# Kernel tuning notes

Hardware: AMD Instinct MI355X
Metric: run time of the kernel (lower is better)

## Reference

```python
import jax, jax.numpy as jnp
import numpy as np

B, N, D, D_OUT = 8, 2048, 256, 256
LN_EPS = 1e-5
LRELU_SLOPE = 0.01


def setup_inputs() -> dict:
    key = jax.random.key(0)
    ks = jax.random.split(key, 11)
    s_in = 1.0 / np.sqrt(D)
    s_out = 1.0 / np.sqrt(D)
    return {
        "x_local": jax.random.normal(ks[0], (B, N, D), dtype=jnp.float32),
        "Wq": jax.random.uniform(ks[1], (D, D), jnp.float32, -s_in, s_in),
        "bq": jax.random.uniform(ks[2], (D,), jnp.float32, -s_in, s_in),
        "Wk": jax.random.uniform(ks[3], (D, D), jnp.float32, -s_in, s_in),
        "bk": jax.random.uniform(ks[4], (D,), jnp.float32, -s_in, s_in),
        "Wv": jax.random.uniform(ks[5], (D, D), jnp.float32, -s_in, s_in),
        "bv": jax.random.uniform(ks[6], (D,), jnp.float32, -s_in, s_in),
        "Wo": jax.random.uniform(ks[7], (D_OUT, D), jnp.float32, -s_out, s_out),
        "bo": jax.random.uniform(ks[8], (D_OUT,), jnp.float32, -s_out, s_out),
        "ln_gamma": jnp.ones((D_OUT,), jnp.float32),
        "ln_beta": jnp.zeros((D_OUT,), jnp.float32),
    }


def reference(x_local, Wq, bq, Wk, bk, Wv, bv, Wo, bo, ln_gamma, ln_beta):
    # Linear layers (torch convention: y = x @ W.T + b)
    Q = jnp.einsum("bnd,ed->bne", x_local, Wq) + bq
    K = jnp.einsum("bnd,ed->bne", x_local, Wk) + bk
    V = jnp.einsum("bnd,ed->bne", x_local, Wv) + bv
    # Unscaled attention (source applies no 1/sqrt(d))
    scores = jnp.einsum("bnd,bmd->bnm", Q, K)          # [B, N, N]
    attn = jax.nn.softmax(scores, axis=-1)
    loc = jnp.einsum("bnm,bmd->bnd", attn, V)           # [B, N, D]
    # fc_out: Linear -> LayerNorm -> LeakyReLU
    h = jnp.einsum("bnd,ed->bne", loc, Wo) + bo          # [B, N, D_OUT]
    mu = jnp.mean(h, axis=-1, keepdims=True)
    var = jnp.mean(jnp.square(h - mu), axis=-1, keepdims=True)
    hn = (h - mu) / jnp.sqrt(var + LN_EPS) * ln_gamma + ln_beta
    return jnp.where(hn >= 0, hn, LRELU_SLOPE * hn)
```

## Files before the change

kernel.cpp:

```cpp
#include <hip/hip_runtime.h>

typedef unsigned short u16;
typedef __attribute__((ext_vector_type(8))) _Float16 f16x8;
typedef __attribute__((ext_vector_type(4))) float f32x4;

#define MFMA_F16 __builtin_amdgcn_mfma_f32_16x16x32_f16

static __device__ __forceinline__ u16 f2h(float f) {
    return __builtin_bit_cast(u16, (_Float16)f);
}
static __device__ __forceinline__ ushort4 f4_to_h4(const float4 v) {
    ushort4 r;
    r.x = f2h(v.x); r.y = f2h(v.y); r.z = f2h(v.z); r.w = f2h(v.w);
    return r;
}
static __device__ __forceinline__ void gl16(const u16* g, u16* l) {
    __builtin_amdgcn_global_load_lds(
        (__attribute__((address_space(1))) void*)(g),
        (__attribute__((address_space(3))) void*)(l),
        16, 0, 0);
}

__global__ __launch_bounds__(256) void prep_w(
    const float* __restrict__ wq, const float* __restrict__ wk,
    const float* __restrict__ wv, const float* __restrict__ wo,
    u16* __restrict__ w4)
{
    const int tid = blockIdx.x * 256 + threadIdx.x;
    for (int i = tid; i < 65536; i += 16384) {
        const float* src = (i < 16384) ? wq : (i < 32768) ? wk
                         : (i < 49152) ? wv : wo;
        ((ushort4*)w4)[i] = f4_to_h4(((const float4*)src)[i & 16383]);
    }
}

__global__ __launch_bounds__(256, 3) void proj_qkv(
    const float* __restrict__ X, const u16* __restrict__ w4,
    const float* __restrict__ bq, const float* __restrict__ bk,
    const float* __restrict__ bv,
    u16* __restrict__ Qh, u16* __restrict__ Kh, u16* __restrict__ Vt)
{
    const int z = blockIdx.y;
    const u16* __restrict__ W     = w4 + z * 65536;
    const float* __restrict__ bias = (z == 0) ? bq : (z == 1) ? bk : bv;

    const int m0   = blockIdx.x * 64;
    const int t    = threadIdx.x;
    const int w    = t >> 6;
    const int lane = t & 63;
    const int quad = lane >> 4;
    const int l16  = lane & 15;

    __shared__ __align__(16) u16 smem[18432];
    u16* Xs = smem;
    u16* Ws = smem + 2560;

    f32x4 acc[16];
#pragma unroll
    for (int i = 0; i < 16; ++i) acc[i] = f32x4{0.f, 0.f, 0.f, 0.f};

    for (int kc = 0; kc < 8; ++kc) {
#pragma unroll
        for (int i = 0; i < 2; ++i) {
            const int ch = i * 256 + t;
            const int row = ch >> 3, cg = ch & 7;
            const float4 v = *(const float4*)&X[(size_t)(m0 + row) * 256 + kc * 32 + cg * 4];
            *(ushort4*)&Xs[row * 40 + cg * 4] = f4_to_h4(v);
        }
#pragma unroll
        for (int i = 0; i < 4; ++i) {
            const int ch = i * 256 + t;
            const int row = ch >> 2, cg = ch & 3;
            *(int4*)&Ws[row * 40 + cg * 8] =
                *(const int4*)&W[(size_t)row * 256 + kc * 32 + cg * 8];
        }
        __syncthreads();

        const f16x8 af = *(const f16x8*)&Xs[(w * 16 + l16) * 40 + quad * 8];
#pragma unroll
        for (int nt = 0; nt < 16; ++nt) {
            const f16x8 bf = *(const f16x8*)&Ws[(nt * 16 + l16) * 40 + quad * 8];
            acc[nt] = MFMA_F16(af, bf, acc[nt], 0, 0, 0);
        }
        __syncthreads();
    }

    if (z < 2) {
        u16* __restrict__ Y = (z == 0) ? Qh : Kh;
#pragma unroll
        for (int nt = 0; nt < 16; ++nt) {
            const int col = nt * 16 + l16;
            const float bb = bias[col];
#pragma unroll
            for (int r = 0; r < 4; ++r)
                smem[(w * 16 + quad * 4 + r) * 264 + col] = f2h(acc[nt][r] + bb);
        }
        __syncthreads();
#pragma unroll
        for (int i = 0; i < 8; ++i) {
            const int ch = i * 256 + t;
            const int row = ch >> 5, cg = ch & 31;
            *(int4*)&Y[(size_t)(m0 + row) * 256 + cg * 8] =
                *(const int4*)&smem[row * 264 + cg * 8];
        }
    } else {
        const int b  = m0 >> 11;
        const int n0 = m0 & 2047;
#pragma unroll
        for (int nt = 0; nt < 16; ++nt) {
            const int col = nt * 16 + l16;
            const float bb = bias[col];
            ushort4 h4;
            h4.x = f2h(acc[nt][0] + bb);
            h4.y = f2h(acc[nt][1] + bb);
            h4.z = f2h(acc[nt][2] + bb);
            h4.w = f2h(acc[nt][3] + bb);
            *(ushort4*)&smem[col * 72 + w * 16 + quad * 4] = h4;
        }
        __syncthreads();
#pragma unroll
        for (int i = 0; i < 8; ++i) {
            const int ch = i * 256 + t;
            const int row = ch >> 3, cg = ch & 7;
            *(int4*)&Vt[(size_t)b * 524288 + (size_t)row * 2048 + n0 + cg * 8] =
                *(const int4*)&smem[row * 72 + cg * 8];
        }
    }
}

__global__ __launch_bounds__(256, 2) void attn(
    const u16* __restrict__ Qh, const u16* __restrict__ Kg,
    const u16* __restrict__ Vt, u16* __restrict__ Op, float* __restrict__ lmp)
{
    const int nz = gridDim.z;
    const int z  = blockIdx.z;
    const int ntiles = 32;
    const int tile0  = ntiles * z;

    const int b  = blockIdx.y;
    const int q0 = blockIdx.x * 64;
    const int t    = threadIdx.x;
    const int w    = t >> 6;
    const int lane = t & 63;
    const int quad = lane >> 4;
    const int l16  = lane & 15;

    __shared__ __align__(16) u16 smem[32768];
    u16* Os = smem;

    f16x8 qf[8];
    {
        const size_t qrow = (size_t)(b * 2048 + q0 + w * 16 + l16) * 256;
#pragma unroll
        for (int kc = 0; kc < 8; ++kc)
            qf[kc] = *(const f16x8*)&Qh[qrow + kc * 32 + quad * 8];
    }

    unsigned kgb[4], vgb[4];
#pragma unroll
    for (int i = 0; i < 4; ++i) {
        const int j  = w * 4 + i;
        const int r  = 2 * j + (lane >> 5);
        const int pr = ((r >> 2) & 3) * 8 + (r >> 4) * 4 + (r & 3);
        const int c  = lane & 31;
        kgb[i] = (unsigned)((b * 2048 + pr) * 256 + ((c ^ (r & 7)) * 8));
        const int rp = 8 * j + (lane >> 3);
        const int c8 = lane & 7;
        const int d  = 2 * rp + (c8 >> 2);
        const int a  = (c8 & 3) ^ (rp & 3);
        vgb[i] = (unsigned)(b * 524288 + d * 2048 + a * 8);
    }

#define STAGE(bufsel, kt_) do {                                              \
        u16* Kb_ = smem + (bufsel) * 16384;                                  \
        u16* Vb_ = Kb_ + 8192;                                               \
        _Pragma("unroll")                                                    \
        for (int i_ = 0; i_ < 4; ++i_) {                                     \
            gl16(Kg + kgb[i_] + (unsigned)(kt_) * 256,                       \
                 Kb_ + (w * 4 + i_) * 512);                                  \
            gl16(Vt + vgb[i_] + (unsigned)(kt_),                             \
                 Vb_ + (w * 4 + i_) * 512);                                  \
        }                                                                    \
    } while (0)

    f32x4 O[16];
#pragma unroll
    for (int i = 0; i < 16; ++i) O[i] = f32x4{0.f, 0.f, 0.f, 0.f};
    float mrow = -1e30f, lrow = 0.f;

    const int vbase = (l16 >> 1) * 64 + (l16 & 1) * 32
                    + ((quad ^ ((l16 >> 1) & 3)) * 8);

    STAGE(0, tile0 * 32);

    for (int it = 0; it < ntiles; ++it) {
        asm volatile("s_waitcnt vmcnt(0)" ::: "memory");
        __builtin_amdgcn_s_barrier();
        __builtin_amdgcn_sched_barrier(0);
        if (it + 1 < ntiles) STAGE((it + 1) & 1, (tile0 + it + 1) * 32);
        __builtin_amdgcn_sched_barrier(0);

        const u16* Kc = smem + (it & 1) * 16384;
        const u16* Vc = Kc + 8192;

        f32x4 S[2];
        S[0] = f32x4{0.f, 0.f, 0.f, 0.f};
        S[1] = f32x4{0.f, 0.f, 0.f, 0.f};
        __builtin_amdgcn_s_setprio(1);
#pragma unroll
        for (int kc = 0; kc < 8; ++kc) {
#pragma unroll
            for (int kn = 0; kn < 2; ++kn) {
                const int r2 = kn * 16 + l16;
                const f16x8 kf = *(const f16x8*)
                    &Kc[r2 * 256 + (((kc * 4 + quad) ^ (l16 & 7)) * 8)];
                S[kn] = MFMA_F16(kf, qf[kc], S[kn], 0, 0, 0);
            }
        }
        __builtin_amdgcn_s_setprio(0);

        float mt = fmaxf(fmaxf(fmaxf(S[0][0], S[0][1]), fmaxf(S[0][2], S[0][3])),
                         fmaxf(fmaxf(S[1][0], S[1][1]), fmaxf(S[1][2], S[1][3])));
        mt = fmaxf(mt, __shfl_xor(mt, 16));
        mt = fmaxf(mt, __shfl_xor(mt, 32));
        if (__any(mt - mrow > 8.f)) {
            const float mnew = fmaxf(mrow, mt);
            const float a = __expf(mrow - mnew);
            lrow *= a;
#pragma unroll
            for (int dv = 0; dv < 16; ++dv)
#pragma unroll
                for (int r = 0; r < 4; ++r) O[dv][r] *= a;
            mrow = mnew;
        }
        f16x8 pfv;
        float s = 0.f;
#pragma unroll
        for (int kn = 0; kn < 2; ++kn)
#pragma unroll
            for (int r = 0; r < 4; ++r) {
                const float e = __expf(S[kn][r] - mrow);
                s += e;
                pfv[kn * 4 + r] = (_Float16)e;
            }
        s += __shfl_xor(s, 16);
        s += __shfl_xor(s, 32);
        lrow += s;

        __builtin_amdgcn_s_setprio(1);
#pragma unroll
        for (int dvt = 0; dvt < 16; ++dvt) {
            const f16x8 vf = *(const f16x8*)&Vc[dvt * 512 + vbase];
            O[dvt] = MFMA_F16(vf, pfv, O[dvt], 0, 0, 0);
        }
        __builtin_amdgcn_s_setprio(0);
    }
#undef STAGE

    __syncthreads();
    {
        const float rl = 1.0f / lrow;
#pragma unroll
        for (int dvt = 0; dvt < 16; ++dvt) {
            ushort4 h4;
            h4.x = f2h(O[dvt][0] * rl);
            h4.y = f2h(O[dvt][1] * rl);
            h4.z = f2h(O[dvt][2] * rl);
            h4.w = f2h(O[dvt][3] * rl);
            *(ushort4*)&Os[(w * 16 + l16) * 264 + dvt * 16 + quad * 4] = h4;
        }
        if (quad == 0) {
            const int grow = b * 2048 + q0 + w * 16 + l16;
            lmp[z * 16384 + grow]        = lrow;
            lmp[(nz + z) * 16384 + grow] = mrow;
        }
    }
    __syncthreads();

    u16* __restrict__ Oz = Op + (size_t)z * 4194304;
    {
        const int row = t >> 2;
#pragma unroll
        for (int i = 0; i < 8; ++i) {
            const int chunk = (t & 3) * 8 + i;
            *(int4*)&Oz[(size_t)(b * 2048 + q0 + row) * 256 + chunk * 8] =
                *(const int4*)&Os[row * 264 + chunk * 8];
        }
    }
}

__global__ __launch_bounds__(256, 2) void outproj_ln(
    const u16* __restrict__ Op, const float* __restrict__ lmp,
    const u16* __restrict__ Woh, const float* __restrict__ bo,
    const float* __restrict__ gamma, const float* __restrict__ beta,
    float* __restrict__ out)
{
    const int m0   = blockIdx.x * 32;
    const int t    = threadIdx.x;
    const int w    = t >> 6;
    const int rw   = w & 1;
    const int cw   = w >> 1;
    const int lane = t & 63;
    const int quad = lane >> 4;
    const int l16  = lane & 15;

    __shared__ __align__(16) u16 Ls[32 * 40];
    __shared__ __align__(16) u16 Ws[256 * 40];
    __shared__ _Float16 wls[2][32];
    __shared__ float part[2][16][2][2];

    if (t < 32) {
        const float l0 = lmp[m0 + t],          l1 = lmp[16384 + m0 + t];
        const float mm0 = lmp[32768 + m0 + t], mm1 = lmp[49152 + m0 + t];
        const float mm = fmaxf(mm0, mm1);
        const float u0 = l0 * __expf(mm0 - mm);
        const float u1 = l1 * __expf(mm1 - mm);
        const float inv = 1.0f / (u0 + u1);
        wls[0][t] = (_Float16)(u0 * inv);
        wls[1][t] = (_Float16)(u1 * inv);
    }
    __syncthreads();

    f32x4 acc[8];
#pragma unroll
    for (int i = 0; i < 8; ++i) acc[i] = f32x4{0.f, 0.f, 0.f, 0.f};

    for (int kc = 0; kc < 8; ++kc) {
        if (t < 128) {
            const int row = t >> 2, cg = t & 3;
            const size_t off = (size_t)(m0 + row) * 256 + kc * 32 + cg * 8;
            const f16x8 o0 = __builtin_bit_cast(f16x8, *(const int4*)&Op[off]);
            const f16x8 o1 = __builtin_bit_cast(f16x8, *(const int4*)&Op[4194304 + off]);
            const _Float16 w0 = wls[0][row], w1 = wls[1][row];
            f16x8 lw;
#pragma unroll
            for (int j = 0; j < 8; ++j) lw[j] = o0[j] * w0 + o1[j] * w1;
            *(int4*)&Ls[row * 40 + cg * 8] = __builtin_bit_cast(int4, lw);
        }
#pragma unroll
        for (int i = 0; i < 4; ++i) {
            const int ch = i * 256 + t;
            const int row = ch >> 2, cg = ch & 3;
            *(int4*)&Ws[row * 40 + cg * 8] =
                *(const int4*)&Woh[(size_t)row * 256 + kc * 32 + cg * 8];
        }
        __syncthreads();

        const f16x8 af = *(const f16x8*)&Ls[(rw * 16 + l16) * 40 + quad * 8];
#pragma unroll
        for (int nt = 0; nt < 8; ++nt) {
            const f16x8 bf = *(const f16x8*)&Ws[((cw * 8 + nt) * 16 + l16) * 40 + quad * 8];
            acc[nt] = MFMA_F16(af, bf, acc[nt], 0, 0, 0);
        }
        __syncthreads();
    }

    float g[8], bt[8], bb[8];
#pragma unroll
    for (int nt = 0; nt < 8; ++nt) {
        const int col = cw * 128 + nt * 16 + l16;
        bb[nt] = bo[col]; g[nt] = gamma[col]; bt[nt] = beta[col];
    }

    float shv[4], sh2v[4];
#pragma unroll
    for (int r = 0; r < 4; ++r) {
        float sh = 0.f, sh2 = 0.f;
#pragma unroll
        for (int nt = 0; nt < 8; ++nt) {
            const float h = acc[nt][r] + bb[nt];
            sh  += h;
            sh2 += h * h;
        }
        sh  += __shfl_xor(sh, 1);  sh  += __shfl_xor(sh, 2);
        sh  += __shfl_xor(sh, 4);  sh  += __shfl_xor(sh, 8);
        sh2 += __shfl_xor(sh2, 1); sh2 += __shfl_xor(sh2, 2);
        sh2 += __shfl_xor(sh2, 4); sh2 += __shfl_xor(sh2, 8);
        shv[r] = sh; sh2v[r] = sh2;
    }
    if (l16 == 0) {
#pragma unroll
        for (int r = 0; r < 4; ++r) {
            part[rw][quad * 4 + r][cw][0] = shv[r];
            part[rw][quad * 4 + r][cw][1] = sh2v[r];
        }
    }
    __syncthreads();

#pragma unroll
    for (int r = 0; r < 4; ++r) {
        const float sh  = shv[r]  + part[rw][quad * 4 + r][cw ^ 1][0];
        const float sh2 = sh2v[r] + part[rw][quad * 4 + r][cw ^ 1][1];
        const float mu  = sh * (1.f / 256.f);
        const float var = fmaxf(sh2 * (1.f / 256.f) - mu * mu, 0.f);
        const float rs  = rsqrtf(var + 1e-5f);
        const size_t row = (size_t)(m0 + rw * 16 + quad * 4 + r) * 256;
#pragma unroll
        for (int nt = 0; nt < 8; ++nt) {
            const float hn = (acc[nt][r] + bb[nt] - mu) * rs * g[nt] + bt[nt];
            out[row + cw * 128 + nt * 16 + l16] = (hn >= 0.f) ? hn : 0.01f * hn;
        }
    }
}

extern "C" void kernel_launch(void* const* d_in, const int* in_sizes, int n_in,
                              void* d_out, int out_size, void* d_ws, size_t ws_size,
                              hipStream_t stream)
{
    const float* x  = (const float*)d_in[0];
    const float* Wq = (const float*)d_in[1];
    const float* bq = (const float*)d_in[2];
    const float* Wk = (const float*)d_in[3];
    const float* bk = (const float*)d_in[4];
    const float* Wv = (const float*)d_in[5];
    const float* bv = (const float*)d_in[6];
    const float* Wo = (const float*)d_in[7];
    const float* bo = (const float*)d_in[8];
    const float* gm = (const float*)d_in[9];
    const float* bt = (const float*)d_in[10];
    float* out = (float*)d_out;

    u16* W4 = (u16*)d_ws;
    u16* Qh = W4 + 262144;
    u16* Kh = Qh + 4194304;
    u16* Vt = Kh + 4194304;
    u16* Op = Vt + 4194304;
    float* lmp = (float*)(Op + 2 * 4194304);
    u16* Woh = W4 + 196608;

    prep_w     <<<64,             256, 0, stream>>>(Wq, Wk, Wv, Wo, W4);
    proj_qkv   <<<dim3(256, 3),   256, 0, stream>>>(x, W4, bq, bk, bv, Qh, Kh, Vt);
    attn       <<<dim3(32, 8, 2), 256, 0, stream>>>(Qh, Kh, Vt, Op, lmp);
    outproj_ln <<<512,            256, 0, stream>>>(Op, lmp, Woh, bo, gm, bt, out);
}
```

Before: 170.7 us.

## Pre-convert X to fp16 and double-buffer QKV projection with async LDS loads

The weight-prep kernel now also converts the fp32 input X to fp16, writing it into the output buffer as scratch, so that proj_qkv no longer converts X inside its loop. proj_qkv replaces its register-staged LDS fills with global_load_lds into a swizzled, double-buffered LDS layout. The next K-chunk is prefetched while MFMAs run on the current one, with one barrier per iteration and raised wave priority during the MFMA loop. This aims to hide global load latency and cut conversion and LDS store work in the projection. The cost is an extra pass over X (read fp32, write fp16) and dependence on the output buffer being free until the last kernel.

```diff
diff --git a/kernel.cpp b/kernel.cpp
--- a/kernel.cpp
+++ b/kernel.cpp
@@ -24,18 +24,24 @@
 __global__ __launch_bounds__(256) void prep_w(
     const float* __restrict__ wq, const float* __restrict__ wk,
     const float* __restrict__ wv, const float* __restrict__ wo,
-    u16* __restrict__ w4)
+    const float* __restrict__ x,
+    u16* __restrict__ w4, u16* __restrict__ xh)
 {
     const int tid = blockIdx.x * 256 + threadIdx.x;
-    for (int i = tid; i < 65536; i += 16384) {
-        const float* src = (i < 16384) ? wq : (i < 32768) ? wk
-                         : (i < 49152) ? wv : wo;
-        ((ushort4*)w4)[i] = f4_to_h4(((const float4*)src)[i & 16383]);
+    {
+        const float* src = (tid < 16384) ? wq : (tid < 32768) ? wk
+                         : (tid < 49152) ? wv : wo;
+        ((ushort4*)w4)[tid] = f4_to_h4(((const float4*)src)[tid & 16383]);
+    }
+#pragma unroll
+    for (int i = 0; i < 16; ++i) {
+        const int j = i * 65536 + tid;
+        ((ushort4*)xh)[j] = f4_to_h4(((const float4*)x)[j]);
     }
 }
 
 __global__ __launch_bounds__(256, 3) void proj_qkv(
-    const float* __restrict__ X, const u16* __restrict__ w4,
+    const u16* __restrict__ Xh, const u16* __restrict__ w4,
     const float* __restrict__ bq, const float* __restrict__ bk,
     const float* __restrict__ bv,
     u16* __restrict__ Qh, u16* __restrict__ Kh, u16* __restrict__ Vt)
@@ -51,39 +57,58 @@
     const int quad = lane >> 4;
     const int l16  = lane & 15;
 
-    __shared__ __align__(16) u16 smem[18432];
-    u16* Xs = smem;
-    u16* Ws = smem + 2560;
+    __shared__ __align__(16) u16 smem[20480];
+
+    const int xrow = t >> 2, xpp = t & 3;
+    const unsigned xsrc = (unsigned)((m0 + xrow) * 256
+                        + ((xpp ^ ((xrow >> 1) & 3)) * 8));
+    unsigned wsrc[4];
+#pragma unroll
+    for (int i = 0; i < 4; ++i) {
+        const int j = i * 256 + t;
+        const int row = j >> 2, p = j & 3;
+        wsrc[i] = (unsigned)(row * 256 + ((p ^ ((row >> 1) & 3)) * 8));
+    }
+
+#define PSTAGE(bufsel, kc_) do {                                             \
+        u16* B_ = smem + (bufsel) * 10240;                                   \
+        gl16(Xh + xsrc + (unsigned)(kc_) * 32, B_ + w * 512);                \
+        _Pragma("unroll")                                                    \
+        for (int i_ = 0; i_ < 4; ++i_)                                       \
+            gl16(W + wsrc[i_] + (unsigned)(kc_) * 32,                        \
+                 B_ + 2048 + i_ * 2048 + w * 512);                           \
+    } while (0)
 
     f32x4 acc[16];
 #pragma unroll
     for (int i = 0; i < 16; ++i) acc[i] = f32x4{0.f, 0.f, 0.f, 0.f};
 
+    const int rp = (quad ^ ((l16 >> 1) & 3)) * 8;
+
+    PSTAGE(0, 0);
+
     for (int kc = 0; kc < 8; ++kc) {
-#pragma unroll
-        for (int i = 0; i < 2; ++i) {
-            const int ch = i * 256 + t;
-            const int row = ch >> 3, cg = ch & 7;
-            const float4 v = *(const float4*)&X[(size_t)(m0 + row) * 256 + kc * 32 + cg * 4];
-            *(ushort4*)&Xs[row * 40 + cg * 4] = f4_to_h4(v);
-        }
-#pragma unroll
-        for (int i = 0; i < 4; ++i) {
-            const int ch = i * 256 + t;
-            const int row = ch >> 2, cg = ch & 3;
-            *(int4*)&Ws[row * 40 + cg * 8] =
-                *(const int4*)&W[(size_t)row * 256 + kc * 32 + cg * 8];
-        }
-        __syncthreads();
-
-        const f16x8 af = *(const f16x8*)&Xs[(w * 16 + l16) * 40 + quad * 8];
+        asm volatile("s_waitcnt vmcnt(0)" ::: "memory");
+        __builtin_amdgcn_s_barrier();
+        __builtin_amdgcn_sched_barrier(0);
+        if (kc + 1 < 8) PSTAGE((kc + 1) & 1, kc + 1);
+        __builtin_amdgcn_sched_barrier(0);
+
+        const u16* Xb = smem + (kc & 1) * 10240;
+        const u16* Wb = Xb + 2048;
+
+        const f16x8 af = *(const f16x8*)&Xb[(w * 16 + l16) * 32 + rp];
+        __builtin_amdgcn_s_setprio(1);
 #pragma unroll
         for (int nt = 0; nt < 16; ++nt) {
-            const f16x8 bf = *(const f16x8*)&Ws[(nt * 16 + l16) * 40 + quad * 8];
+            const f16x8 bf = *(const f16x8*)&Wb[(nt * 16 + l16) * 32 + rp];
             acc[nt] = MFMA_F16(af, bf, acc[nt], 0, 0, 0);
         }
-        __syncthreads();
-    }
+        __builtin_amdgcn_s_setprio(0);
+    }
+#undef PSTAGE
+
+    __syncthreads();
 
     if (z < 2) {
         u16* __restrict__ Y = (z == 0) ? Qh : Kh;
@@ -164,10 +189,10 @@
         const int pr = ((r >> 2) & 3) * 8 + (r >> 4) * 4 + (r & 3);
         const int c  = lane & 31;
         kgb[i] = (unsigned)((b * 2048 + pr) * 256 + ((c ^ (r & 7)) * 8));
-        const int rp = 8 * j + (lane >> 3);
+        const int rp2 = 8 * j + (lane >> 3);
         const int c8 = lane & 7;
-        const int d  = 2 * rp + (c8 >> 2);
-        const int a  = (c8 & 3) ^ (rp & 3);
+        const int d  = 2 * rp2 + (c8 >> 2);
+        const int a  = (c8 & 3) ^ (rp2 & 3);
         vgb[i] = (unsigned)(b * 524288 + d * 2048 + a * 8);
     }
 
@@ -427,9 +452,10 @@
     u16* Op = Vt + 4194304;
     float* lmp = (float*)(Op + 2 * 4194304);
     u16* Woh = W4 + 196608;
-
-    prep_w     <<<64,             256, 0, stream>>>(Wq, Wk, Wv, Wo, W4);
-    proj_qkv   <<<dim3(256, 3),   256, 0, stream>>>(x, W4, bq, bk, bv, Qh, Kh, Vt);
+    u16* Xh  = (u16*)d_out;
+
+    prep_w     <<<256,            256, 0, stream>>>(Wq, Wk, Wv, Wo, x, W4, Xh);
+    proj_qkv   <<<dim3(256, 3),   256, 0, stream>>>(Xh, W4, bq, bk, bv, Qh, Kh, Vt);
     attn       <<<dim3(32, 8, 2), 256, 0, stream>>>(Qh, Kh, Vt, Op, lmp);
     outproj_ln <<<512,            256, 0, stream>>>(Op, lmp, Woh, bo, gm, bt, out);
 }
```

New measurement: 167.3 us. -2.0%, faster.
